# Optimization experiments

Measured on AMD Instinct MI355X. Metric: run time of the kernel, lower is better.

Reference implementation:

```python
import jax, jax.numpy as jnp
import numpy as np
from jax import lax

# Static problem sizes (see shape_source)
B, C, N = 32, 512, 64
SENTS_PER_VIDEO = 4
TARGETS_PER_SENT = 2
S = B * SENTS_PER_VIDEO          # 128 sentences
M = S * TARGETS_PER_SENT         # 256 target moments
P = N * (N + 1) // 2             # 2080 valid proposals (upper-tri mask2d)
T_TEMP = 0.1
MARGIN = 0.0
NEG_IOU = 0.5
K_TOP = 1                        # pos_topk
WEIGHT = 1.0


def setup_inputs() -> dict:
    key = jax.random.key(0)
    k1, k2, k3, k4 = jax.random.split(key, 4)
    return {
        "video_feats": jax.random.normal(k1, (B, C, N, N), jnp.float32),
        "sents_feats": jax.random.normal(k2, (S, C), jnp.float32),
        "num_sentences": jnp.full((B,), SENTS_PER_VIDEO, jnp.int32),
        "num_targets": jnp.full((S,), TARGETS_PER_SENT, jnp.int32),
        "iou2d": jax.random.uniform(k3, (S, N, N), jnp.float32),
        "iou2ds": jax.random.uniform(k4, (M, N, N), jnp.float32),
        "mask2d": jnp.triu(jnp.ones((N, N), bool)),
        "epoch": 0,  # < start_DNS_epoch -> DNS branch skipped
    }


def _log_cross_entropy(pos_scores, all_scores, neg_mask, t, m):
    # Faithful to LogCrossEntropy.forward
    pos_exp = jnp.exp((pos_scores - m) / t)
    neg_exp_sum = jnp.sum(jnp.exp(all_scores / t) * neg_mask, axis=-1)
    loss = -((pos_scores - m) / t - jnp.log(pos_exp + neg_exp_sum))
    return jnp.mean(loss)


def _l2_normalize(x, axis=-1, eps=1e-12):
    n = jnp.linalg.norm(x, axis=axis, keepdims=True)
    return x / jnp.maximum(n, eps)


def reference(video_feats, sents_feats, num_sentences, num_targets,
              iou2d, iou2ds, mask2d, epoch):
    # Compact valid proposals (P is static: upper-triangular mask2d)
    idx = jnp.nonzero(mask2d.reshape(-1), size=P)[0]              # (P,)
    v = video_feats.reshape(B, C, N * N)[:, :, idx]               # (B,C,P)
    v = jnp.transpose(v, (0, 2, 1))                               # (B,P,C)
    iou2d_f = iou2d.reshape(S, N * N)[:, idx]                     # (S,P)
    iou2ds_f = iou2ds.reshape(M, N * N)[:, idx]                   # (M,P)

    v = _l2_normalize(v)
    sents = _l2_normalize(sents_feats)

    scatter_s2v = jnp.repeat(jnp.arange(B), num_sentences, total_repeat_length=S)
    scatter_m2s = jnp.repeat(jnp.arange(S), num_targets, total_repeat_length=M)
    scatter_m2v = scatter_s2v[scatter_m2s]

    # top-K proposals per target moment by IoU
    topk_idx = lax.top_k(iou2ds_f, K_TOP)[1]                      # (M,K)
    topk_v = jnp.take_along_axis(v[scatter_m2v], topk_idx[:, :, None], axis=1)  # (M,K,C)

    # inter-video loss
    inter_video_pos = jnp.einsum('mkc,mc->mk', topk_v, sents[scatter_m2s])  # (M,K)
    inter_video_all = jnp.einsum('mkc,sc->mks', topk_v, sents)              # (M,K,S)
    inter_video_neg_mask = (~jnp.eye(S, dtype=bool))[scatter_m2s][:, None, :]  # (M,1,S)
    loss_inter_video = _log_cross_entropy(
        inter_video_pos, inter_video_all, inter_video_neg_mask, T_TEMP, MARGIN)

    # inter-query loss
    inter_query_pos = inter_video_pos                              # (M,K)
    inter_query_all = (sents @ v.reshape(B * P, C).T)[:, None, :]  # (S,1,B*P)
    # pos_mask: block-diagonal per video, refined by IoU > neg_iou inside own block
    onehot = jnp.eye(B, dtype=bool)[scatter_s2v]                   # (S,B)
    pos_mask = (onehot[:, :, None] & (iou2d_f > NEG_IOU)[:, None, :]).reshape(S, B * P)
    inter_query_neg_mask = (~pos_mask)[:, None, :]                 # (S,1,B*P)
    loss_inter_query = _log_cross_entropy(
        inter_query_pos, inter_query_all[scatter_m2s],
        inter_query_neg_mask[scatter_m2s], T_TEMP, MARGIN)

    total = (loss_inter_video + loss_inter_query) * WEIGHT
    return total, loss_inter_video, loss_inter_query
```

## Files before the change

kernel.cpp:

```cpp
#include <hip/hip_runtime.h>
#include <cstdint>

#define BB 32
#define CC 512
#define NSQ 4096
#define SS 128
#define MM 256
#define PP 2080
#define JJ (BB*PP)
#define NBIG (JJ/128)

#define WS_SN     0
#define WS_SNB    262144
#define WS_IDX    393216
#define WS_IV     401536
#define WS_NEGQ   532608

typedef short bf16x8 __attribute__((ext_vector_type(8)));
typedef float f32x4  __attribute__((ext_vector_type(4)));

__device__ __forceinline__ unsigned short f2bf(float x) {
    unsigned int u = __float_as_uint(x);
    unsigned int r = (u + 0x7fffu + ((u >> 16) & 1u)) >> 16;
    return (unsigned short)r;
}

__global__ void k_prep(const float* __restrict__ sents, float* __restrict__ sn,
                       unsigned short* __restrict__ snb,
                       int* __restrict__ idx, float* __restrict__ negq) {
    const int blk = blockIdx.x, t = threadIdx.x;
    if (blk < 128) {
        __shared__ float red[256];
        const float* row = sents + (size_t)blk * CC;
        float x0 = row[t], x1 = row[t + 256];
        red[t] = x0 * x0 + x1 * x1;
        __syncthreads();
        for (int off = 128; off > 0; off >>= 1) {
            if (t < off) red[t] += red[t + off];
            __syncthreads();
        }
        float rn = 1.0f / fmaxf(sqrtf(red[0]), 1e-12f);
        float y0 = x0 * rn, y1 = x1 * rn;
        sn[(size_t)blk * CC + t]        = y0;
        sn[(size_t)blk * CC + t + 256]  = y1;
        snb[(size_t)blk * CC + t]       = f2bf(y0);
        snb[(size_t)blk * CC + t + 256] = f2bf(y1);
    } else if (blk < 144) {
        int i = (blk - 128) * 256 + t;
        int r = i >> 6, c = i & 63;
        if (c >= r) {
            int p = r * 64 - (r * (r - 1)) / 2 + (c - r);
            idx[p] = i;
        }
    } else {
        if (t < 128) negq[t] = 0.0f;
    }
}


union SMem {
    struct {
        unsigned short sA[128 * 64];
        unsigned short vB[128 * 64];
        int   colb[128];
        int   colflat[128];
        float colrn[128];
        float sqpart[256];
    } big;
    struct {
        float sv[256];
        int   si[256];
        float tvs[512];
        float red[256];
    } fus;
};

__global__ __launch_bounds__(256, 4)
void k_mega(const float* __restrict__ video, const float* __restrict__ sn,
            const unsigned short* __restrict__ snb,
            const float* __restrict__ iou2d, const float* __restrict__ iou2ds,
            const int* __restrict__ idx,
            float* __restrict__ iv, float* __restrict__ negq) {
    __shared__ SMem sm;
    const int t = threadIdx.x;

    if (blockIdx.x < MM) {
        const int m = blockIdx.x;
        {
            float best = -1e30f; int bi = 1 << 30;
            const float* row = iou2ds + (size_t)m * NSQ;
            for (int p = t; p < PP; p += 256) {
                float v = row[idx[p]];
                if (v > best || (v == best && p < bi)) { best = v; bi = p; }
            }
            sm.fus.sv[t] = best; sm.fus.si[t] = bi;
            __syncthreads();
            for (int off = 128; off > 0; off >>= 1) {
                if (t < off) {
                    float v2 = sm.fus.sv[t + off]; int i2 = sm.fus.si[t + off];
                    if (v2 > sm.fus.sv[t] || (v2 == sm.fus.sv[t] && i2 < sm.fus.si[t])) {
                        sm.fus.sv[t] = v2; sm.fus.si[t] = i2;
                    }
                }
                __syncthreads();
            }
        }
        const int flat = idx[sm.fus.si[0]];
        const int b = m >> 3;

        const float* base = video + (size_t)b * CC * NSQ + flat;
        float x0 = base[(size_t)t * NSQ];
        float x1 = base[(size_t)(t + 256) * NSQ];
        sm.fus.red[t] = x0 * x0 + x1 * x1;
        __syncthreads();
        for (int off = 128; off > 0; off >>= 1) {
            if (t < off) sm.fus.red[t] += sm.fus.red[t + off];
            __syncthreads();
        }
        float rn = 1.0f / fmaxf(sqrtf(sm.fus.red[0]), 1e-12f);
        sm.fus.tvs[t] = x0 * rn;
        sm.fus.tvs[t + 256] = x1 * rn;
        __syncthreads();

        const int s = t & 127, h = t >> 7;
        const float4* a4 = (const float4*)(sm.fus.tvs + h * 256);
        const float4* b4 = (const float4*)(sn + (size_t)s * CC + h * 256);
        float acc = 0.f;
#pragma unroll 8
        for (int c = 0; c < 64; c++) {
            float4 a = a4[c], bb = b4[c];
            acc += a.x * bb.x + a.y * bb.y + a.z * bb.z + a.w * bb.w;
        }
        __syncthreads();
        sm.fus.red[t] = acc;
        __syncthreads();
        if (t < 128) iv[(size_t)m * SS + t] = sm.fus.red[t] + sm.fus.red[t + 128];
        return;
    }

    const int w    = t >> 6;
    const int lane = t & 63;
    const int q    = lane >> 4;
    const int l15  = lane & 15;
    const int j0   = (blockIdx.x - MM) * 128;

    if (t < 128) {
        int col = j0 + t;
        int b = col / PP;
        sm.big.colb[t] = b;
        sm.big.colflat[t] = idx[col - b * PP];
    }

    const int jj = t & 127;
    const int kh = t >> 7;
    int colL = j0 + jj;
    int bL = colL / PP;
    int flatL = idx[colL - bL * PP];
    const float* vbase = video + (size_t)bL * (CC * NSQ) + flatL;

    f32x4 acc[2][8];
#pragma unroll
    for (int i = 0; i < 2; i++)
#pragma unroll
        for (int j = 0; j < 8; j++) acc[i][j] = (f32x4){0.f, 0.f, 0.f, 0.f};

    float sqa = 0.f;
    const int swzA_w = jj & 7;
    (void)swzA_w;

    for (int k0 = 0; k0 < CC; k0 += 64) {
        __syncthreads();
#pragma unroll
        for (int it = 0; it < 4; it++) {
            int lin = t + it * 256;
            int row = lin >> 3, G = lin & 7;
            bf16x8 v = *(const bf16x8*)(snb + (size_t)row * CC + k0 + G * 8);
            *(bf16x8*)(sm.big.sA + row * 64 + ((G ^ (row & 7)) * 8)) = v;
        }
        {
            const float* vp = vbase + (size_t)(k0 + kh * 32) * NSQ;
#pragma unroll
            for (int g = 0; g < 4; g++) {
                unsigned short buf[8];
#pragma unroll
                for (int i = 0; i < 8; i++) {
                    float x = vp[(size_t)(g * 8 + i) * NSQ];
                    sqa += x * x;
                    buf[i] = f2bf(x);
                }
                int G = kh * 4 + g;
                *(bf16x8*)(sm.big.vB + jj * 64 + ((G ^ (jj & 7)) * 8)) = *(bf16x8*)buf;
            }
        }
        __syncthreads();
#pragma unroll
        for (int ks = 0; ks < 64; ks += 32) {
            const int so = ((q + (ks >> 3)) ^ (l15 & 7)) * 8;
            bf16x8 a[2], bfr[8];
#pragma unroll
            for (int rt = 0; rt < 2; rt++) {
                int row = w * 32 + rt * 16 + l15;
                a[rt] = *(const bf16x8*)(sm.big.sA + row * 64 + so);
            }
#pragma unroll
            for (int ct = 0; ct < 8; ct++) {
                int col = ct * 16 + l15;
                bfr[ct] = *(const bf16x8*)(sm.big.vB + col * 64 + so);
            }
#pragma unroll
            for (int rt = 0; rt < 2; rt++)
#pragma unroll
                for (int ct = 0; ct < 8; ct++)
                    acc[rt][ct] = __builtin_amdgcn_mfma_f32_16x16x32_bf16(
                        a[rt], bfr[ct], acc[rt][ct], 0, 0, 0);
        }
    }

    sm.big.sqpart[t] = sqa;
    __syncthreads();
    if (t < 128)
        sm.big.colrn[t] = 1.0f / fmaxf(sqrtf(sm.big.sqpart[t] + sm.big.sqpart[t + 128]), 1e-12f);
    __syncthreads();

#pragma unroll
    for (int rt = 0; rt < 2; rt++) {
#pragma unroll
        for (int r = 0; r < 4; r++) {
            int s = w * 32 + rt * 16 + q * 4 + r;
            float rowsum = 0.f;
#pragma unroll
            for (int ct = 0; ct < 8; ct++) {
                int c = ct * 16 + l15;
                float sc = acc[rt][ct][r] * sm.big.colrn[c];
                float e = __expf(sc * 10.0f);
                if ((s >> 2) == sm.big.colb[c]) {
                    if (iou2d[(size_t)s * NSQ + sm.big.colflat[c]] > 0.5f) e = 0.f;
                }
                rowsum += e;
            }
#pragma unroll
            for (int msk = 1; msk < 16; msk <<= 1)
                rowsum += __shfl_xor(rowsum, msk, 64);
            if (l15 == 0) atomicAdd(&negq[s], rowsum);
        }
    }
}

__global__ void k_final(const float* __restrict__ iv, const float* __restrict__ negq,
                        float* __restrict__ out) {
    const int t = threadIdx.x;
    __shared__ float rv[256], rq[256];
    const float* row = iv + (size_t)t * SS;
    const int ms = t >> 1;
    float pos = row[ms];
    float nv = 0.f;
    for (int s = 0; s < SS; s++) {
        float e = expf(row[s] * 10.0f);
        if (s == ms) e = 0.f;
        nv += e;
    }
    float pe = expf(pos * 10.0f);
    float lv = logf(pe + nv) - pos * 10.0f;
    float lq = logf(pe + negq[ms]) - pos * 10.0f;
    rv[t] = lv; rq[t] = lq;
    __syncthreads();
    for (int off = 128; off > 0; off >>= 1) {
        if (t < off) { rv[t] += rv[t + off]; rq[t] += rq[t + off]; }
        __syncthreads();
    }
    if (t == 0) {
        float liv = rv[0] / 256.f, liq = rq[0] / 256.f;
        out[0] = liv + liq;
        out[1] = liv;
        out[2] = liq;
    }
}

extern "C" void kernel_launch(void* const* d_in, const int* in_sizes, int n_in,
                              void* d_out, int out_size, void* d_ws, size_t ws_size,
                              hipStream_t stream) {
    const float* video  = (const float*)d_in[0];
    const float* sents  = (const float*)d_in[1];
    const float* iou2d  = (const float*)d_in[4];
    const float* iou2ds = (const float*)d_in[5];
    float* out = (float*)d_out;

    char* ws = (char*)d_ws;
    float*          sn   = (float*)(ws + WS_SN);
    unsigned short* snb  = (unsigned short*)(ws + WS_SNB);
    int*            idx  = (int*)(ws + WS_IDX);
    float*          iv   = (float*)(ws + WS_IV);
    float*          negq = (float*)(ws + WS_NEGQ);

    k_prep <<<145, 256, 0, stream>>>(sents, sn, snb, idx, negq);
    k_mega <<<MM + NBIG, 256, 0, stream>>>(video, sn, snb, iou2d, iou2ds, idx, iv, negq);
    k_final<<<1, 256, 0, stream>>>(iv, negq, out);
}
```

Before: 489.6 us.

## Register-prefetch next K tile during MFMA and replace atomics with partial sums

```diff
diff --git a/kernel.cpp b/kernel.cpp
--- a/kernel.cpp
+++ b/kernel.cpp
@@ -14,7 +14,7 @@
 #define WS_SNB    262144
 #define WS_IDX    393216
 #define WS_IV     401536
-#define WS_NEGQ   532608
+#define WS_PART   532608
 
 typedef short bf16x8 __attribute__((ext_vector_type(8)));
 typedef float f32x4  __attribute__((ext_vector_type(4)));
@@ -26,8 +26,7 @@
 }
 
 __global__ void k_prep(const float* __restrict__ sents, float* __restrict__ sn,
-                       unsigned short* __restrict__ snb,
-                       int* __restrict__ idx, float* __restrict__ negq) {
+                       unsigned short* __restrict__ snb, int* __restrict__ idx) {
     const int blk = blockIdx.x, t = threadIdx.x;
     if (blk < 128) {
         __shared__ float red[256];
@@ -45,15 +44,13 @@
         sn[(size_t)blk * CC + t + 256]  = y1;
         snb[(size_t)blk * CC + t]       = f2bf(y0);
         snb[(size_t)blk * CC + t + 256] = f2bf(y1);
-    } else if (blk < 144) {
+    } else {
         int i = (blk - 128) * 256 + t;
         int r = i >> 6, c = i & 63;
         if (c >= r) {
             int p = r * 64 - (r * (r - 1)) / 2 + (c - r);
             idx[p] = i;
         }
-    } else {
-        if (t < 128) negq[t] = 0.0f;
     }
 }
 
@@ -75,12 +72,12 @@
     } fus;
 };
 
-__global__ __launch_bounds__(256, 4)
+__global__ __launch_bounds__(256, 2)
 void k_mega(const float* __restrict__ video, const float* __restrict__ sn,
             const unsigned short* __restrict__ snb,
             const float* __restrict__ iou2d, const float* __restrict__ iou2ds,
             const int* __restrict__ idx,
-            float* __restrict__ iv, float* __restrict__ negq) {
+            float* __restrict__ iv, float* __restrict__ part) {
     __shared__ SMem sm;
     const int t = threadIdx.x;
 
@@ -142,7 +139,8 @@
     const int lane = t & 63;
     const int q    = lane >> 4;
     const int l15  = lane & 15;
-    const int j0   = (blockIdx.x - MM) * 128;
+    const int bid  = blockIdx.x - MM;
+    const int j0   = bid * 128;
 
     if (t < 128) {
         int col = j0 + t;
@@ -151,12 +149,28 @@
         sm.big.colflat[t] = idx[col - b * PP];
     }
 
+    const int G_    = t & 7;
+    const int rowA0 = t >> 3;
+    const int swzA  = ((G_ ^ (rowA0 & 7)) * 8);
     const int jj = t & 127;
     const int kh = t >> 7;
     int colL = j0 + jj;
     int bL = colL / PP;
     int flatL = idx[colL - bL * PP];
-    const float* vbase = video + (size_t)bL * (CC * NSQ) + flatL;
+    const float* vbase = video + (size_t)bL * (CC * NSQ) + flatL
+                               + (size_t)(kh * 32) * NSQ;
+    const unsigned short* snbA = snb + (size_t)rowA0 * CC + G_ * 8;
+    unsigned short* sAp = sm.big.sA + rowA0 * 64 + swzA;
+    unsigned short* vBp = sm.big.vB + jj * 64;
+    const int jj7 = jj & 7;
+
+    bf16x8 prA[4];
+    float  pr[32];
+#pragma unroll
+    for (int it = 0; it < 4; it++)
+        prA[it] = *(const bf16x8*)(snbA + (size_t)it * 32 * CC);
+#pragma unroll
+    for (int i = 0; i < 32; i++) pr[i] = vbase[(size_t)i * NSQ];
 
     f32x4 acc[2][8];
 #pragma unroll
@@ -165,37 +179,38 @@
         for (int j = 0; j < 8; j++) acc[i][j] = (f32x4){0.f, 0.f, 0.f, 0.f};
 
     float sqa = 0.f;
-    const int swzA_w = jj & 7;
-    (void)swzA_w;
 
     for (int k0 = 0; k0 < CC; k0 += 64) {
-        __syncthreads();
-#pragma unroll
-        for (int it = 0; it < 4; it++) {
-            int lin = t + it * 256;
-            int row = lin >> 3, G = lin & 7;
-            bf16x8 v = *(const bf16x8*)(snb + (size_t)row * CC + k0 + G * 8);
-            *(bf16x8*)(sm.big.sA + row * 64 + ((G ^ (row & 7)) * 8)) = v;
-        }
-        {
-            const float* vp = vbase + (size_t)(k0 + kh * 32) * NSQ;
-#pragma unroll
-            for (int g = 0; g < 4; g++) {
-                unsigned short buf[8];
-#pragma unroll
-                for (int i = 0; i < 8; i++) {
-                    float x = vp[(size_t)(g * 8 + i) * NSQ];
-                    sqa += x * x;
-                    buf[i] = f2bf(x);
-                }
-                int G = kh * 4 + g;
-                *(bf16x8*)(sm.big.vB + jj * 64 + ((G ^ (jj & 7)) * 8)) = *(bf16x8*)buf;
-            }
-        }
-        __syncthreads();
+#pragma unroll
+        for (int it = 0; it < 4; it++)
+            *(bf16x8*)(sAp + it * 32 * 64) = prA[it];
+#pragma unroll
+        for (int g = 0; g < 4; g++) {
+            unsigned short buf[8];
+#pragma unroll
+            for (int i = 0; i < 8; i++) {
+                float x = pr[g * 8 + i];
+                sqa += x * x;
+                buf[i] = f2bf(x);
+            }
+            int Gb = kh * 4 + g;
+            *(bf16x8*)(vBp + ((Gb ^ jj7) * 8)) = *(bf16x8*)buf;
+        }
+        __syncthreads();
+
+        if (k0 + 64 < CC) {
+            const int kn = k0 + 64;
+#pragma unroll
+            for (int it = 0; it < 4; it++)
+                prA[it] = *(const bf16x8*)(snbA + (size_t)it * 32 * CC + kn);
+            const float* vp = vbase + (size_t)kn * NSQ;
+#pragma unroll
+            for (int i = 0; i < 32; i++) pr[i] = vp[(size_t)i * NSQ];
+        }
+
 #pragma unroll
         for (int ks = 0; ks < 64; ks += 32) {
-            const int so = ((q + (ks >> 3)) ^ (l15 & 7)) * 8;
+            const int so = (((ks >> 3) + q) ^ (l15 & 7)) * 8;
             bf16x8 a[2], bfr[8];
 #pragma unroll
             for (int rt = 0; rt < 2; rt++) {
@@ -214,6 +229,7 @@
                     acc[rt][ct] = __builtin_amdgcn_mfma_f32_16x16x32_bf16(
                         a[rt], bfr[ct], acc[rt][ct], 0, 0, 0);
         }
+        __syncthreads();
     }
 
     sm.big.sqpart[t] = sqa;
@@ -222,6 +238,14 @@
         sm.big.colrn[t] = 1.0f / fmaxf(sqrtf(sm.big.sqpart[t] + sm.big.sqpart[t + 128]), 1e-12f);
     __syncthreads();
 
+    float crn[8]; int cb[8], cf[8];
+#pragma unroll
+    for (int ct = 0; ct < 8; ct++) {
+        int c = ct * 16 + l15;
+        crn[ct] = sm.big.colrn[c];
+        cb[ct]  = sm.big.colb[c];
+        cf[ct]  = sm.big.colflat[c];
+    }
 #pragma unroll
     for (int rt = 0; rt < 2; rt++) {
 #pragma unroll
@@ -230,26 +254,33 @@
             float rowsum = 0.f;
 #pragma unroll
             for (int ct = 0; ct < 8; ct++) {
-                int c = ct * 16 + l15;
-                float sc = acc[rt][ct][r] * sm.big.colrn[c];
+                float sc = acc[rt][ct][r] * crn[ct];
                 float e = __expf(sc * 10.0f);
-                if ((s >> 2) == sm.big.colb[c]) {
-                    if (iou2d[(size_t)s * NSQ + sm.big.colflat[c]] > 0.5f) e = 0.f;
+                if ((s >> 2) == cb[ct]) {
+                    if (iou2d[(size_t)s * NSQ + cf[ct]] > 0.5f) e = 0.f;
                 }
                 rowsum += e;
             }
 #pragma unroll
             for (int msk = 1; msk < 16; msk <<= 1)
                 rowsum += __shfl_xor(rowsum, msk, 64);
-            if (l15 == 0) atomicAdd(&negq[s], rowsum);
-        }
-    }
-}
-
-__global__ void k_final(const float* __restrict__ iv, const float* __restrict__ negq,
+            if (l15 == 0) part[(size_t)bid * 128 + s] = rowsum;
+        }
+    }
+}
+
+__global__ void k_final(const float* __restrict__ iv, const float* __restrict__ part,
                         float* __restrict__ out) {
     const int t = threadIdx.x;
+    __shared__ float nqs[256];
     __shared__ float rv[256], rq[256];
+    {
+        const int sl = t & 127, h = t >> 7;
+        float nq = 0.f;
+        for (int j = h; j < NBIG; j += 2) nq += part[(size_t)j * 128 + sl];
+        nqs[t] = nq;
+    }
+    __syncthreads();
     const float* row = iv + (size_t)t * SS;
     const int ms = t >> 1;
     float pos = row[ms];
@@ -260,8 +291,9 @@
         nv += e;
     }
     float pe = expf(pos * 10.0f);
+    float negq_ms = nqs[ms] + nqs[ms + 128];
     float lv = logf(pe + nv) - pos * 10.0f;
-    float lq = logf(pe + negq[ms]) - pos * 10.0f;
+    float lq = logf(pe + negq_ms) - pos * 10.0f;
     rv[t] = lv; rq[t] = lq;
     __syncthreads();
     for (int off = 128; off > 0; off >>= 1) {
@@ -290,9 +322,9 @@
     unsigned short* snb  = (unsigned short*)(ws + WS_SNB);
     int*            idx  = (int*)(ws + WS_IDX);
     float*          iv   = (float*)(ws + WS_IV);
-    float*          negq = (float*)(ws + WS_NEGQ);
-
-    k_prep <<<145, 256, 0, stream>>>(sents, sn, snb, idx, negq);
-    k_mega <<<MM + NBIG, 256, 0, stream>>>(video, sn, snb, iou2d, iou2ds, idx, iv, negq);
-    k_final<<<1, 256, 0, stream>>>(iv, negq, out);
-}
+    float*          part = (float*)(ws + WS_PART);
+
+    k_prep <<<144, 256, 0, stream>>>(sents, sn, snb, idx);
+    k_mega <<<MM + NBIG, 256, 0, stream>>>(video, sn, snb, iou2d, iou2ds, idx, iv, part);
+    k_final<<<1, 256, 0, stream>>>(iv, part, out);
+}
```

After: 481.2 us. No clear change (-1.7%).
